# Performance work log

Measured on AMD Instinct MI355X. Metric: run time of the kernel, lower is better.

The kernel has to match this reference:

```python
import jax, jax.numpy as jnp
import numpy as np

B, OBS, L, D, BINS, HID = 4096, 128, 4, 8, 16, 512
S = L * D  # max_seq_len = 32; qchunk_size = S, single Q chunk


def _lin(k, i, o, s):
    kw, kb = jax.random.split(k)
    return jax.random.normal(kw, (i, o), jnp.float32) * s, jnp.zeros((o,), jnp.float32)


def setup_inputs() -> dict:
    key = jax.random.key(0)
    ks = jax.random.split(key, 12)
    inp = {
        "obs": jax.random.normal(ks[0], (B, OBS), jnp.float32),
        "category": jax.random.randint(ks[1], (B, L, D), 0, BINS, jnp.int32),
    }
    # v_network: obs_dim -> 512 -> 512 -> 512 -> 1 (tanh hidden)
    dims_v = [OBS, HID, HID, HID, 1]
    for i in range(4):
        w, b = _lin(ks[2 + i], dims_v[i], dims_v[i + 1], 0.05)
        inp[f"v_w{i}"], inp[f"v_b{i}"] = w, b
    # q_network: (obs_dim+actor_dim) -> 512 -> 512 -> 512 -> bins*S
    dims_q = [OBS + D, HID, HID, HID, BINS * S]
    for i in range(4):
        w, b = _lin(ks[6 + i], dims_q[i], dims_q[i + 1], 0.05)
        inp[f"q_w{i}"], inp[f"q_b{i}"] = w, b
    return inp


def _mlp(x, ws, bs):
    for w, b in zip(ws[:-1], bs[:-1]):
        x = jnp.tanh(x @ w + b)
    return x @ ws[-1] + bs[-1]


def _actions_from_category(category):
    # zoom_in per (level, dim): width_l = 2/bins^(l+1); low accumulates cat*width.
    cat = category.astype(jnp.float32)  # (B, L, D)
    widths = 2.0 / (jnp.float32(BINS) ** jnp.arange(1, L + 1, dtype=jnp.float32))  # (L,)
    cum_low = jnp.cumsum(cat * widths[None, :, None], axis=1)  # (B, L, D)
    mids = -1.0 + cum_low + 0.5 * widths[None, :, None]  # midpoint after each level
    # mids_full[:, j, d] = midpoint of dim d after j zoom-in updates (j=0 -> 0.0)
    mids_full = jnp.concatenate(
        [jnp.zeros((category.shape[0], 1, D), jnp.float32), mids], axis=1)  # (B, L+1, D)
    # at sequence step k (input to Q), dim d' has had U[k,d'] updates
    k = jnp.arange(S)
    U = k[:, None] // D + (jnp.arange(D)[None, :] < (k[:, None] % D)).astype(jnp.int32)  # (S, D)
    dgrid = jnp.broadcast_to(jnp.arange(D)[None, :], (S, D))
    return mids_full[:, U, dgrid]  # (B, S, D)


def reference(obs, category,
              v_w0, v_b0, v_w1, v_b1, v_w2, v_b2, v_w3, v_b3,
              q_w0, q_b0, q_w1, q_b1, q_w2, q_b2, q_w3, q_b3):
    vw = [v_w0, v_w1, v_w2, v_w3]; vb = [v_b0, v_b1, v_b2, v_b3]
    qw = [q_w0, q_w1, q_w2, q_w3]; qb = [q_b0, q_b1, q_b2, q_b3]
    b = obs.shape[0]
    actions = _actions_from_category(category)  # (B, S, D)
    obs_rep = jnp.broadcast_to(obs[:, None, :], (b, S, OBS))
    x = jnp.concatenate([obs_rep, actions], axis=-1)  # (B, S, OBS+D)
    adv = _mlp(x, qw, qb)  # (B, S, S*BINS)
    adv = adv.reshape(b, S, S, BINS)
    s_idx = jnp.arange(S)
    adv = adv[:, s_idx, s_idx, :]  # diagonal gather -> (B, S, BINS)
    adv = adv.reshape(b, L, D, BINS)
    value = _mlp(obs, vw, vb)  # (B, 1)
    nbias = jnp.zeros((b, L, D, 1), jnp.float32)  # use_nbias=False
    return value, adv, nbias
```

## Files before the change

### kernel.cpp

```cpp
#include <hip/hip_runtime.h>
#include <hip/hip_bf16.h>

#define B_SZ   4096
#define OBS_N  128
#define HID    512


typedef __bf16 bf16x8_t __attribute__((ext_vector_type(8)));
typedef float  f32x4_t  __attribute__((ext_vector_type(4)));

__device__ inline float fast_tanh(float x) {
    float e = __builtin_amdgcn_exp2f(x * 2.885390081777927f);
    return fmaf(-2.f, __builtin_amdgcn_rcpf(e + 1.f), 1.f);
}

__device__ inline void gld_lds16(const void* g, void* l) {
    __builtin_amdgcn_global_load_lds(
        (const __attribute__((address_space(1))) void*)g,
        (__attribute__((address_space(3))) void*)l, 16, 0, 0);
}

__device__ inline int hs_off(int row, int col) {
    int c = col >> 3;
    int phys = (c & ~7) | ((c ^ (row & 7)) & 7);
    return row * 512 + phys * 8 + (col & 7);
}

__global__ __launch_bounds__(256) void prep_kernel(
    const float* __restrict__ obs, const int* __restrict__ category,
    const float* __restrict__ qw0, const float* __restrict__ qw1,
    const float* __restrict__ qw2, const float* __restrict__ qw3,
    const float* __restrict__ vw0, const float* __restrict__ vw1,
    const float* __restrict__ vw2,
    __hip_bfloat16* __restrict__ obs_bf,
    __hip_bfloat16* __restrict__ w0t, __hip_bfloat16* __restrict__ w1t,
    __hip_bfloat16* __restrict__ w2t, __hip_bfloat16* __restrict__ w3t,
    __hip_bfloat16* __restrict__ vw0t, __hip_bfloat16* __restrict__ vw1t,
    __hip_bfloat16* __restrict__ vw2t,
    float* __restrict__ acts, float* __restrict__ nbias)
{
    const int bid = blockIdx.x, tid = threadIdx.x;
    if (bid < 2048) {
        int i = bid * 256 + tid;
        obs_bf[i] = __float2bfloat16(obs[i]);
    } else if (bid < 2560) {
        const float* src = (bid < 2304) ? qw0 : vw0;
        __hip_bfloat16* dst = (bid < 2304) ? w0t : vw0t;
        int idx = ((bid - 2048) & 255) * 256 + tid;
        int n = idx >> 7, k = idx & 127;
        dst[idx] = __float2bfloat16(src[k * 512 + n]);
    } else if (bid < 7680) {
        int job = (bid - 2560) >> 10;
        const float* srcs[5] = {qw1, qw2, qw3, vw1, vw2};
        __hip_bfloat16* dsts[5] = {w1t, w2t, w3t, vw1t, vw2t};
        int idx = ((bid - 2560) & 1023) * 256 + tid;
        int e    = idx & 7;
        int lane = (idx >> 3) & 63;
        int kc   = (idx >> 9) & 15;
        int tile = idx >> 13;
        int k = kc * 32 + (lane >> 4) * 8 + e;
        int n = tile * 16 + (lane & 15);
        dsts[job][idx] = __float2bfloat16(srcs[job][k * 512 + n]);
    } else if (bid < 11776) {
        int t = (bid - 7680) * 256 + tid;
        int d = t & 7;
        int r = t >> 3;
        int b = r & 4095, s = r >> 12;
        int U = (s >> 3) + ((d < (s & 7)) ? 1 : 0);
        float a = 0.f;
        if (U > 0) {
            float w = 0.125f, cum = 0.f;
            for (int j = 0; j < U; ++j) {
                cum += (float)category[b * 32 + j * 8 + d] * w;
                if (j == U - 1) a = -1.f + cum + 0.5f * w;
                w *= 0.0625f;
            }
        }
        acts[t] = a;
    } else {
        int i = (bid - 11776) * 256 + tid;
        nbias[i] = 0.f;
    }
}

__global__ __launch_bounds__(256) void gemm_dual(
    const __hip_bfloat16* __restrict__ A0, const __hip_bfloat16* __restrict__ B0,
    const float* __restrict__ bias0, void* __restrict__ C0, int K0, int epi0, int nb0,
    const __hip_bfloat16* __restrict__ A1, const __hip_bfloat16* __restrict__ B1,
    const float* __restrict__ bias1, void* __restrict__ C1, int K1, int epi1)
{
    __shared__ __hip_bfloat16 As[128 * 32];
    __shared__ __hip_bfloat16 Bs[128 * 32];

    const __hip_bfloat16 *A, *Bt;
    const float* bias;
    void* Cout;
    int K, epi, tb;
    if ((int)blockIdx.x < nb0) {
        A = A0; Bt = B0; bias = bias0; Cout = C0; K = K0; epi = epi0; tb = blockIdx.x;
    } else {
        A = A1; Bt = B1; bias = bias1; Cout = C1; K = K1; epi = epi1; tb = blockIdx.x - nb0;
    }
    const long m0 = (long)(tb >> 2) * 128;
    const int  n0 = (tb & 3) * 128;

    const int tid  = threadIdx.x;
    const int wave = tid >> 6, lane = tid & 63;
    const int quad = lane >> 4, t = lane & 15;
    const int wr = wave >> 1, wc = wave & 1;

    f32x4_t acc[4][4] = {};

    const int lrow  = lane >> 2;
    const int lkoff = (((lane & 3) + (lane >> 3)) & 3) * 8;

    const __hip_bfloat16* Ag0 = A  + (m0 + wave * 32 +      lrow) * (long)K + lkoff;
    const __hip_bfloat16* Ag1 = A  + (m0 + wave * 32 + 16 + lrow) * (long)K + lkoff;
    const __hip_bfloat16* Bg0 = Bt + (long)(n0 + wave * 32 +      lrow) * K + lkoff;
    const __hip_bfloat16* Bg1 = Bt + (long)(n0 + wave * 32 + 16 + lrow) * K + lkoff;
    __hip_bfloat16* AsB0 = &As[(wave * 32) * 32];
    __hip_bfloat16* AsB1 = &As[(wave * 32 + 16) * 32];
    __hip_bfloat16* BsB0 = &Bs[(wave * 32) * 32];
    __hip_bfloat16* BsB1 = &Bs[(wave * 32 + 16) * 32];

    const int slot = ((quad - (t >> 1)) & 3) * 8;

    for (int k0 = 0; k0 < K; k0 += 32) {
        gld_lds16(Ag0 + k0, AsB0);
        gld_lds16(Ag1 + k0, AsB1);
        gld_lds16(Bg0 + k0, BsB0);
        gld_lds16(Bg1 + k0, BsB1);
        __syncthreads();
        bf16x8_t af[4], bfr[4];
        #pragma unroll
        for (int i = 0; i < 4; ++i)
            af[i] = *(const bf16x8_t*)&As[(wr * 64 + i * 16 + t) * 32 + slot];
        #pragma unroll
        for (int j = 0; j < 4; ++j)
            bfr[j] = *(const bf16x8_t*)&Bs[(wc * 64 + j * 16 + t) * 32 + slot];
        #pragma unroll
        for (int i = 0; i < 4; ++i)
            #pragma unroll
            for (int j = 0; j < 4; ++j)
                acc[i][j] = __builtin_amdgcn_mfma_f32_16x16x32_bf16(af[i], bfr[j], acc[i][j], 0, 0, 0);
        __syncthreads();
    }

    #pragma unroll
    for (int i = 0; i < 4; ++i) {
        const long rbase = m0 + wr * 64 + i * 16 + quad * 4;
        #pragma unroll
        for (int j = 0; j < 4; ++j) {
            const int col = n0 + wc * 64 + j * 16 + t;
            #pragma unroll
            for (int r = 0; r < 4; ++r) {
                float v = acc[i][j][r];
                if (epi == 1) {
                    v = fast_tanh(v + bias[col]);
                    ((__hip_bfloat16*)Cout)[(rbase + r) * 512 + col] = __float2bfloat16(v);
                } else if (epi == 2) {
                    ((__hip_bfloat16*)Cout)[(rbase + r) * 512 + col] = __float2bfloat16(v);
                } else {
                    ((float*)Cout)[(rbase + r) * 512 + col] = v;
                }
            }
        }
    }
}

__device__ inline void mfma_layer(
    __hip_bfloat16* hs, const __hip_bfloat16* __restrict__ Wt,
    const float* __restrict__ bias, int w, int lane)
{
    const int quad = lane >> 4, t = lane & 15;
    const int n0w = w * 64;
    const __hip_bfloat16* Wl = Wt + ((size_t)(w * 4) * 16 * 64 + lane) * 8;
    f32x4_t acc[4][4] = {};
    bf16x8_t wc[4], wn[4], ac[4];
    #pragma unroll
    for (int j = 0; j < 4; ++j)
        wc[j] = *(const bf16x8_t*)(Wl + (size_t)(j * 16) * 512);

    #pragma unroll 2
    for (int kc = 0; kc < 16; ++kc) {
        const int craw = kc * 4 + quad;
        const int phys = (craw & ~7) | ((craw ^ (t & 7)) & 7);
        #pragma unroll
        for (int rt = 0; rt < 4; ++rt)
            ac[rt] = *(const bf16x8_t*)&hs[(rt * 16 + t) * 512 + phys * 8];
        if (kc < 15) {
            #pragma unroll
            for (int j = 0; j < 4; ++j)
                wn[j] = *(const bf16x8_t*)(Wl + (size_t)(j * 16 + kc + 1) * 512);
        }
        #pragma unroll
        for (int j = 0; j < 4; ++j)
            #pragma unroll
            for (int rt = 0; rt < 4; ++rt)
                acc[rt][j] = __builtin_amdgcn_mfma_f32_16x16x32_bf16(wc[j], ac[rt], acc[rt][j], 0, 0, 0);
        #pragma unroll
        for (int j = 0; j < 4; ++j) wc[j] = wn[j];
    }
    __syncthreads();
    #pragma unroll
    for (int j = 0; j < 4; ++j) {
        const int oc0 = n0w + j * 16 + quad * 4;
        const float4 bl = *(const float4*)&bias[oc0];
        const int cbase = oc0 >> 3;
        const int sub = (quad & 1) * 4;
        #pragma unroll
        for (int rt = 0; rt < 4; ++rt) {
            const int row = rt * 16 + t;
            union { __hip_bfloat16 b[4]; uint2 v; } o;
            o.b[0] = __float2bfloat16(fast_tanh(acc[rt][j][0] + bl.x));
            o.b[1] = __float2bfloat16(fast_tanh(acc[rt][j][1] + bl.y));
            o.b[2] = __float2bfloat16(fast_tanh(acc[rt][j][2] + bl.z));
            o.b[3] = __float2bfloat16(fast_tanh(acc[rt][j][3] + bl.w));
            const int phys = (cbase & ~7) | ((cbase ^ (row & 7)) & 7);
            *(uint2*)&hs[row * 512 + phys * 8 + sub] = o.v;
        }
    }
    __syncthreads();
}

__global__ __launch_bounds__(512, 4) void fused_kernel(
    const __hip_bfloat16* __restrict__ p_bf,
    const __hip_bfloat16* __restrict__ pv_bf,
    const float* __restrict__ acts,
    const float* __restrict__ qw0, const float* __restrict__ qb0,
    const __hip_bfloat16* __restrict__ w1t, const float* __restrict__ qb1,
    const __hip_bfloat16* __restrict__ w2t, const float* __restrict__ qb2,
    const __hip_bfloat16* __restrict__ w3t, const float* __restrict__ qb3,
    float* __restrict__ advout,
    const float* __restrict__ vb0,
    const __hip_bfloat16* __restrict__ vw1t, const float* __restrict__ vb1,
    const __hip_bfloat16* __restrict__ vw2t, const float* __restrict__ vb2,
    const float* __restrict__ vw3, const float* __restrict__ vb3,
    float* __restrict__ vout)
{
    __shared__ __hip_bfloat16 hs[64 * 512];
    const int bid = blockIdx.x;
    const int tid = threadIdx.x;
    const int w = tid >> 6, lane = tid & 63;
    const int quad = lane >> 4, t = lane & 15;
    const bool is_q = bid < 2048;
    const int s  = is_q ? (bid >> 6) : 0;
    const int mb = is_q ? (bid & 63) : (bid - 2048);

    {
        const int col0 = lane * 8;
        float bb[8];
        {
            const float* bsrc = is_q ? qb0 : vb0;
            float4 b0 = *(const float4*)&bsrc[col0];
            float4 b1 = *(const float4*)&bsrc[col0 + 4];
            bb[0] = b0.x; bb[1] = b0.y; bb[2] = b0.z; bb[3] = b0.w;
            bb[4] = b1.x; bb[5] = b1.y; bb[6] = b1.z; bb[7] = b1.w;
        }
        if (is_q) {
            float wr[8][8];
            #pragma unroll
            for (int d = 0; d < 8; ++d) {
                float4 u0 = *(const float4*)&qw0[(128 + d) * 512 + col0];
                float4 u1 = *(const float4*)&qw0[(128 + d) * 512 + col0 + 4];
                wr[d][0] = u0.x; wr[d][1] = u0.y; wr[d][2] = u0.z; wr[d][3] = u0.w;
                wr[d][4] = u1.x; wr[d][5] = u1.y; wr[d][6] = u1.z; wr[d][7] = u1.w;
            }
            for (int i = 0; i < 8; ++i) {
                const int row = w * 8 + i;
                const int b = mb * 64 + row;
                const long r = (long)s * 4096 + b;
                union { bf16x8_t vec; __hip_bfloat16 e[8]; } pu;
                pu.vec = *(const bf16x8_t*)&p_bf[(size_t)b * 512 + col0];
                float4 a0 = *(const float4*)&acts[r * 8];
                float4 a1 = *(const float4*)&acts[r * 8 + 4];
                float a[8] = {a0.x, a0.y, a0.z, a0.w, a1.x, a1.y, a1.z, a1.w};
                float v[8];
                #pragma unroll
                for (int cc = 0; cc < 8; ++cc) v[cc] = __bfloat162float(pu.e[cc]) + bb[cc];
                #pragma unroll
                for (int d = 0; d < 8; ++d)
                    #pragma unroll
                    for (int cc = 0; cc < 8; ++cc)
                        v[cc] = fmaf(a[d], wr[d][cc], v[cc]);
                union { bf16x8_t vec; __hip_bfloat16 e[8]; } o;
                #pragma unroll
                for (int cc = 0; cc < 8; ++cc) o.e[cc] = __float2bfloat16(fast_tanh(v[cc]));
                const int phys = (lane & ~7) | ((lane ^ (row & 7)) & 7);
                *(bf16x8_t*)&hs[row * 512 + phys * 8] = o.vec;
            }
        } else {
            for (int i = 0; i < 8; ++i) {
                const int row = w * 8 + i;
                const int b = mb * 64 + row;
                union { bf16x8_t vec; __hip_bfloat16 e[8]; } pu;
                pu.vec = *(const bf16x8_t*)&pv_bf[(size_t)b * 512 + col0];
                union { bf16x8_t vec; __hip_bfloat16 e[8]; } o;
                #pragma unroll
                for (int cc = 0; cc < 8; ++cc)
                    o.e[cc] = __float2bfloat16(fast_tanh(__bfloat162float(pu.e[cc]) + bb[cc]));
                const int phys = (lane & ~7) | ((lane ^ (row & 7)) & 7);
                *(bf16x8_t*)&hs[row * 512 + phys * 8] = o.vec;
            }
        }
    }
    __syncthreads();

    mfma_layer(hs, is_q ? w1t : vw1t, is_q ? qb1 : vb1, w, lane);
    mfma_layer(hs, is_q ? w2t : vw2t, is_q ? qb2 : vb2, w, lane);

    if (is_q) {
        if (w < 4) {
            const __hip_bfloat16* W3l = w3t + ((size_t)s * 16 * 64 + (size_t)lane) * 8;
            f32x4_t acc = {};
            #pragma unroll 4
            for (int kc = 0; kc < 16; ++kc) {
                const int craw = kc * 4 + quad;
                const int phys = (craw & ~7) | ((craw ^ (t & 7)) & 7);
                bf16x8_t a = *(const bf16x8_t*)&hs[(w * 16 + t) * 512 + phys * 8];
                bf16x8_t bq = *(const bf16x8_t*)(W3l + (size_t)kc * 512);
                acc = __builtin_amdgcn_mfma_f32_16x16x32_bf16(a, bq, acc, 0, 0, 0);
            }
            const float bias3 = qb3[s * 16 + t];
            #pragma unroll
            for (int rr = 0; rr < 4; ++rr) {
                const int row = w * 16 + quad * 4 + rr;
                const int b = mb * 64 + row;
                advout[(size_t)b * 512 + s * 16 + t] = acc[rr] + bias3;
            }
        }
    } else {
        const int row = tid >> 3, seg = tid & 7;
        float sum = 0.f;
        for (int k = seg * 64; k < seg * 64 + 64; ++k)
            sum += __bfloat162float(hs[hs_off(row, k)]) * vw3[k];
        sum += __shfl_xor(sum, 1);
        sum += __shfl_xor(sum, 2);
        sum += __shfl_xor(sum, 4);
        if (seg == 0) vout[mb * 64 + row] = sum + vb3[0];
    }
}

extern "C" void kernel_launch(void* const* d_in, const int* in_sizes, int n_in,
                              void* d_out, int out_size, void* d_ws, size_t ws_size,
                              hipStream_t stream) {
    const float* obs      = (const float*)d_in[0];
    const int*   category = (const int*)d_in[1];
    const float* v_w0 = (const float*)d_in[2];
    const float* v_b0 = (const float*)d_in[3];
    const float* v_w1 = (const float*)d_in[4];
    const float* v_b1 = (const float*)d_in[5];
    const float* v_w2 = (const float*)d_in[6];
    const float* v_b2 = (const float*)d_in[7];
    const float* v_w3 = (const float*)d_in[8];
    const float* v_b3 = (const float*)d_in[9];
    const float* q_w0 = (const float*)d_in[10];
    const float* q_b0 = (const float*)d_in[11];
    const float* q_w1 = (const float*)d_in[12];
    const float* q_b1 = (const float*)d_in[13];
    const float* q_w2 = (const float*)d_in[14];
    const float* q_b2 = (const float*)d_in[15];
    const float* q_w3 = (const float*)d_in[16];
    const float* q_b3 = (const float*)d_in[17];

    char* ws = (char*)d_ws;
    __hip_bfloat16* obs_bf = (__hip_bfloat16*)(ws + 0);
    __hip_bfloat16* w0t    = (__hip_bfloat16*)(ws + 1048576);
    __hip_bfloat16* vw0t   = (__hip_bfloat16*)(ws + 1179648);
    __hip_bfloat16* w1t    = (__hip_bfloat16*)(ws + 1310720);
    __hip_bfloat16* w2t    = (__hip_bfloat16*)(ws + 1835008);
    __hip_bfloat16* w3t    = (__hip_bfloat16*)(ws + 2359296);
    __hip_bfloat16* vw1t   = (__hip_bfloat16*)(ws + 2883584);
    __hip_bfloat16* vw2t   = (__hip_bfloat16*)(ws + 3407872);
    float*          acts   = (float*)         (ws + 3932160);
    __hip_bfloat16* p_bf   = (__hip_bfloat16*)(ws + 8126464);
    __hip_bfloat16* pv_bf  = (__hip_bfloat16*)(ws + 12320768);

    float* out       = (float*)d_out;
    float* out_value = out;
    float* out_adv   = out + 4096;
    float* out_nbias = out + 4096 + (size_t)B_SZ * 512;

    prep_kernel<<<12288, 256, 0, stream>>>(
        obs, category, q_w0, q_w1, q_w2, q_w3, v_w0, v_w1, v_w2,
        obs_bf, w0t, w1t, w2t, w3t, vw0t, vw1t, vw2t, acts, out_nbias);

    gemm_dual<<<256, 256, 0, stream>>>(
        obs_bf, w0t, nullptr, p_bf, 128, 2, 128,
        obs_bf, vw0t, nullptr, pv_bf, 128, 2);

    fused_kernel<<<2112, 512, 0, stream>>>(
        p_bf, pv_bf, acts, q_w0, q_b0, w1t, q_b1, w2t, q_b2, w3t, q_b3, out_adv,
        v_b0, vw1t, v_b1, vw2t, v_b2, v_w3, v_b3, out_value);
}
```

Before: 283.9 us.

## Compute first-layer action and bias term with MFMA using augmented weights

The first Q/V layer epilogue used a scalar 8x8 FMA loop over action features plus a bias add. It now runs a single MFMA with an augmented K dimension: the 8 action weights, plus a bias row multiplied by a constant 1.0 lane. The accumulator is seeded from the fp32 obs projection, written as fp32 instead of bf16. This moves per-element VALU work onto matrix units and keeps the projection in higher precision, at the cost of doubling the p/pv buffer traffic read per block (fp32 vs bf16) and extra prep work for the augmented weights and bf16 actions.

```diff
diff --git a/kernel.cpp b/kernel.cpp
--- a/kernel.cpp
+++ b/kernel.cpp
@@ -28,16 +28,18 @@
 
 __global__ __launch_bounds__(256) void prep_kernel(
     const float* __restrict__ obs, const int* __restrict__ category,
-    const float* __restrict__ qw0, const float* __restrict__ qw1,
-    const float* __restrict__ qw2, const float* __restrict__ qw3,
-    const float* __restrict__ vw0, const float* __restrict__ vw1,
-    const float* __restrict__ vw2,
+    const float* __restrict__ qw0, const float* __restrict__ qb0,
+    const float* __restrict__ qw1, const float* __restrict__ qw2,
+    const float* __restrict__ qw3,
+    const float* __restrict__ vw0, const float* __restrict__ vb0,
+    const float* __restrict__ vw1, const float* __restrict__ vw2,
     __hip_bfloat16* __restrict__ obs_bf,
     __hip_bfloat16* __restrict__ w0t, __hip_bfloat16* __restrict__ w1t,
     __hip_bfloat16* __restrict__ w2t, __hip_bfloat16* __restrict__ w3t,
     __hip_bfloat16* __restrict__ vw0t, __hip_bfloat16* __restrict__ vw1t,
     __hip_bfloat16* __restrict__ vw2t,
-    float* __restrict__ acts, float* __restrict__ nbias)
+    __hip_bfloat16* __restrict__ w0aug, __hip_bfloat16* __restrict__ vw0aug,
+    __hip_bfloat16* __restrict__ acts_bf, float* __restrict__ nbias)
 {
     const int bid = blockIdx.x, tid = threadIdx.x;
     if (bid < 2048) {
@@ -76,9 +78,27 @@
                 w *= 0.0625f;
             }
         }
-        acts[t] = a;
+        acts_bf[t] = __float2bfloat16(a);
+    } else if (bid < 11904) {
+        int sub = bid - 11776;
+        bool isv = sub >= 64;
+        int idx = (sub & 63) * 256 + tid;
+        int e    = idx & 7;
+        int lane = (idx >> 3) & 63;
+        int tile = idx >> 9;
+        int k = (lane >> 4) * 8 + e;
+        int n = tile * 16 + (lane & 15);
+        float v = 0.f;
+        if (!isv) {
+            if (k < 8) v = qw0[(128 + k) * 512 + n];
+            else if (k == 8) v = qb0[n];
+            w0aug[idx] = __float2bfloat16(v);
+        } else {
+            if (k == 8) v = vb0[n];
+            vw0aug[idx] = __float2bfloat16(v);
+        }
     } else {
-        int i = (bid - 11776) * 256 + tid;
+        int i = (bid - 11904) * 256 + tid;
         nbias[i] = 0.f;
     }
 }
@@ -164,6 +184,31 @@
                     ((float*)Cout)[(rbase + r) * 512 + col] = v;
                 }
             }
+        }
+    }
+}
+
+__device__ inline void epi_store(
+    __hip_bfloat16* hs, f32x4_t acc[4][4], const float* bias,
+    int n0w, int quad, int t)
+{
+    #pragma unroll
+    for (int j = 0; j < 4; ++j) {
+        const int oc0 = n0w + j * 16 + quad * 4;
+        float4 bl = {0.f, 0.f, 0.f, 0.f};
+        if (bias) bl = *(const float4*)&bias[oc0];
+        const int cbase = oc0 >> 3;
+        const int sub = (quad & 1) * 4;
+        #pragma unroll
+        for (int rt = 0; rt < 4; ++rt) {
+            const int row = rt * 16 + t;
+            union { __hip_bfloat16 b[4]; uint2 v; } o;
+            o.b[0] = __float2bfloat16(fast_tanh(acc[rt][j][0] + bl.x));
+            o.b[1] = __float2bfloat16(fast_tanh(acc[rt][j][1] + bl.y));
+            o.b[2] = __float2bfloat16(fast_tanh(acc[rt][j][2] + bl.z));
+            o.b[3] = __float2bfloat16(fast_tanh(acc[rt][j][3] + bl.w));
+            const int phys = (cbase & ~7) | ((cbase ^ (row & 7)) & 7);
+            *(uint2*)&hs[row * 512 + phys * 8 + sub] = o.v;
         }
     }
 }
@@ -202,37 +247,20 @@
         for (int j = 0; j < 4; ++j) wc[j] = wn[j];
     }
     __syncthreads();
-    #pragma unroll
-    for (int j = 0; j < 4; ++j) {
-        const int oc0 = n0w + j * 16 + quad * 4;
-        const float4 bl = *(const float4*)&bias[oc0];
-        const int cbase = oc0 >> 3;
-        const int sub = (quad & 1) * 4;
-        #pragma unroll
-        for (int rt = 0; rt < 4; ++rt) {
-            const int row = rt * 16 + t;
-            union { __hip_bfloat16 b[4]; uint2 v; } o;
-            o.b[0] = __float2bfloat16(fast_tanh(acc[rt][j][0] + bl.x));
-            o.b[1] = __float2bfloat16(fast_tanh(acc[rt][j][1] + bl.y));
-            o.b[2] = __float2bfloat16(fast_tanh(acc[rt][j][2] + bl.z));
-            o.b[3] = __float2bfloat16(fast_tanh(acc[rt][j][3] + bl.w));
-            const int phys = (cbase & ~7) | ((cbase ^ (row & 7)) & 7);
-            *(uint2*)&hs[row * 512 + phys * 8 + sub] = o.v;
-        }
-    }
+    epi_store(hs, acc, bias, n0w, quad, t);
     __syncthreads();
 }
 
 __global__ __launch_bounds__(512, 4) void fused_kernel(
-    const __hip_bfloat16* __restrict__ p_bf,
-    const __hip_bfloat16* __restrict__ pv_bf,
-    const float* __restrict__ acts,
-    const float* __restrict__ qw0, const float* __restrict__ qb0,
+    const float* __restrict__ p,
+    const float* __restrict__ pv,
+    const __hip_bfloat16* __restrict__ acts_bf,
+    const __hip_bfloat16* __restrict__ w0aug,
+    const __hip_bfloat16* __restrict__ vw0aug,
     const __hip_bfloat16* __restrict__ w1t, const float* __restrict__ qb1,
     const __hip_bfloat16* __restrict__ w2t, const float* __restrict__ qb2,
     const __hip_bfloat16* __restrict__ w3t, const float* __restrict__ qb3,
     float* __restrict__ advout,
-    const float* __restrict__ vb0,
     const __hip_bfloat16* __restrict__ vw1t, const float* __restrict__ vb1,
     const __hip_bfloat16* __restrict__ vw2t, const float* __restrict__ vb2,
     const float* __restrict__ vw3, const float* __restrict__ vb3,
@@ -246,63 +274,42 @@
     const bool is_q = bid < 2048;
     const int s  = is_q ? (bid >> 6) : 0;
     const int mb = is_q ? (bid & 63) : (bid - 2048);
+    const int n0w = w * 64;
 
     {
-        const int col0 = lane * 8;
-        float bb[8];
-        {
-            const float* bsrc = is_q ? qb0 : vb0;
-            float4 b0 = *(const float4*)&bsrc[col0];
-            float4 b1 = *(const float4*)&bsrc[col0 + 4];
-            bb[0] = b0.x; bb[1] = b0.y; bb[2] = b0.z; bb[3] = b0.w;
-            bb[4] = b1.x; bb[5] = b1.y; bb[6] = b1.z; bb[7] = b1.w;
-        }
-        if (is_q) {
-            float wr[8][8];
-            #pragma unroll
-            for (int d = 0; d < 8; ++d) {
-                float4 u0 = *(const float4*)&qw0[(128 + d) * 512 + col0];
-                float4 u1 = *(const float4*)&qw0[(128 + d) * 512 + col0 + 4];
-                wr[d][0] = u0.x; wr[d][1] = u0.y; wr[d][2] = u0.z; wr[d][3] = u0.w;
-                wr[d][4] = u1.x; wr[d][5] = u1.y; wr[d][6] = u1.z; wr[d][7] = u1.w;
+        const float* P = is_q ? p : pv;
+        const __hip_bfloat16* W0 = is_q ? w0aug : vw0aug;
+        f32x4_t acc[4][4];
+        #pragma unroll
+        for (int rt = 0; rt < 4; ++rt) {
+            const float* Prow = &P[(size_t)(mb * 64 + rt * 16 + t) * 512 + n0w + quad * 4];
+            #pragma unroll
+            for (int j = 0; j < 4; ++j)
+                acc[rt][j] = *(const f32x4_t*)(Prow + j * 16);
+        }
+        bf16x8_t bfrag[4];
+        #pragma unroll
+        for (int rt = 0; rt < 4; ++rt) {
+            union { bf16x8_t vec; unsigned short u[8]; } bu;
+            #pragma unroll
+            for (int i = 0; i < 8; ++i) bu.u[i] = 0;
+            if (quad == 1) bu.u[0] = 0x3F80;
+            if (is_q && quad == 0) {
+                const long r = (long)s * 4096 + mb * 64 + rt * 16 + t;
+                bu.vec = *(const bf16x8_t*)&acts_bf[r * 8];
             }
-            for (int i = 0; i < 8; ++i) {
-                const int row = w * 8 + i;
-                const int b = mb * 64 + row;
-                const long r = (long)s * 4096 + b;
-                union { bf16x8_t vec; __hip_bfloat16 e[8]; } pu;
-                pu.vec = *(const bf16x8_t*)&p_bf[(size_t)b * 512 + col0];
-                float4 a0 = *(const float4*)&acts[r * 8];
-                float4 a1 = *(const float4*)&acts[r * 8 + 4];
-                float a[8] = {a0.x, a0.y, a0.z, a0.w, a1.x, a1.y, a1.z, a1.w};
-                float v[8];
-                #pragma unroll
-                for (int cc = 0; cc < 8; ++cc) v[cc] = __bfloat162float(pu.e[cc]) + bb[cc];
-                #pragma unroll
-                for (int d = 0; d < 8; ++d)
-                    #pragma unroll
-                    for (int cc = 0; cc < 8; ++cc)
-                        v[cc] = fmaf(a[d], wr[d][cc], v[cc]);
-                union { bf16x8_t vec; __hip_bfloat16 e[8]; } o;
-                #pragma unroll
-                for (int cc = 0; cc < 8; ++cc) o.e[cc] = __float2bfloat16(fast_tanh(v[cc]));
-                const int phys = (lane & ~7) | ((lane ^ (row & 7)) & 7);
-                *(bf16x8_t*)&hs[row * 512 + phys * 8] = o.vec;
-            }
-        } else {
-            for (int i = 0; i < 8; ++i) {
-                const int row = w * 8 + i;
-                const int b = mb * 64 + row;
-                union { bf16x8_t vec; __hip_bfloat16 e[8]; } pu;
-                pu.vec = *(const bf16x8_t*)&pv_bf[(size_t)b * 512 + col0];
-                union { bf16x8_t vec; __hip_bfloat16 e[8]; } o;
-                #pragma unroll
-                for (int cc = 0; cc < 8; ++cc)
-                    o.e[cc] = __float2bfloat16(fast_tanh(__bfloat162float(pu.e[cc]) + bb[cc]));
-                const int phys = (lane & ~7) | ((lane ^ (row & 7)) & 7);
-                *(bf16x8_t*)&hs[row * 512 + phys * 8] = o.vec;
-            }
-        }
+            bfrag[rt] = bu.vec;
+        }
+        bf16x8_t wq[4];
+        #pragma unroll
+        for (int j = 0; j < 4; ++j)
+            wq[j] = *(const bf16x8_t*)(W0 + ((size_t)(w * 4 + j) * 64 + lane) * 8);
+        #pragma unroll
+        for (int j = 0; j < 4; ++j)
+            #pragma unroll
+            for (int rt = 0; rt < 4; ++rt)
+                acc[rt][j] = __builtin_amdgcn_mfma_f32_16x16x32_bf16(wq[j], bfrag[rt], acc[rt][j], 0, 0, 0);
+        epi_store(hs, acc, nullptr, n0w, quad, t);
     }
     __syncthreads();
 
@@ -372,24 +379,27 @@
     __hip_bfloat16* w3t    = (__hip_bfloat16*)(ws + 2359296);
     __hip_bfloat16* vw1t   = (__hip_bfloat16*)(ws + 2883584);
     __hip_bfloat16* vw2t   = (__hip_bfloat16*)(ws + 3407872);
-    float*          acts   = (float*)         (ws + 3932160);
-    __hip_bfloat16* p_bf   = (__hip_bfloat16*)(ws + 8126464);
-    __hip_bfloat16* pv_bf  = (__hip_bfloat16*)(ws + 12320768);
+    __hip_bfloat16* w0aug  = (__hip_bfloat16*)(ws + 3932160);
+    __hip_bfloat16* vw0aug = (__hip_bfloat16*)(ws + 3964928);
+    __hip_bfloat16* acts_bf= (__hip_bfloat16*)(ws + 3997696);
+    float*          p      = (float*)         (ws + 6094848);
+    float*          pv     = (float*)         (ws + 14483456);
 
     float* out       = (float*)d_out;
     float* out_value = out;
     float* out_adv   = out + 4096;
     float* out_nbias = out + 4096 + (size_t)B_SZ * 512;
 
-    prep_kernel<<<12288, 256, 0, stream>>>(
-        obs, category, q_w0, q_w1, q_w2, q_w3, v_w0, v_w1, v_w2,
-        obs_bf, w0t, w1t, w2t, w3t, vw0t, vw1t, vw2t, acts, out_nbias);
+    prep_kernel<<<12416, 256, 0, stream>>>(
+        obs, category, q_w0, q_b0, q_w1, q_w2, q_w3, v_w0, v_b0, v_w1, v_w2,
+        obs_bf, w0t, w1t, w2t, w3t, vw0t, vw1t, vw2t, w0aug, vw0aug,
+        acts_bf, out_nbias);
 
     gemm_dual<<<256, 256, 0, stream>>>(
-        obs_bf, w0t, nullptr, p_bf, 128, 2, 128,
-        obs_bf, vw0t, nullptr, pv_bf, 128, 2);
+        obs_bf, w0t, nullptr, p, 128, 0, 128,
+        obs_bf, vw0t, nullptr, pv, 128, 0);
 
     fused_kernel<<<2112, 512, 0, stream>>>(
-        p_bf, pv_bf, acts, q_w0, q_b0, w1t, q_b1, w2t, q_b2, w3t, q_b3, out_adv,
-        v_b0, vw1t, v_b1, vw2t, v_b2, v_w3, v_b3, out_value);
-}
+        p, pv, acts_bf, w0aug, vw0aug, w1t, q_b1, w2t, q_b2, w3t, q_b3, out_adv,
+        vw1t, v_b1, vw2t, v_b2, v_w3, v_b3, out_value);
+}
```

Measured after the change: 278.5 us. No clear change (-1.9%).
